# Optimization experiments

Hardware: AMD Instinct MI355X
Metric: run time of the kernel (lower is better)

Reference implementation:

```python
import jax, jax.numpy as jnp
import numpy as np

DIM = 256
DH = 32
HEADS = DIM // DH
AG = 6      # agent_size
WS = 7      # window_size
N = AG * WS * WS  # 294 tokens per window


def _rel_index():
    ws = (AG, WS, WS)
    coords = np.stack(np.meshgrid(np.arange(ws[0]), np.arange(ws[1]), np.arange(ws[2]), indexing='ij'))
    flat = coords.reshape(3, -1)                      # (3, N)
    rel = flat[:, :, None] - flat[:, None, :]         # (3, N, N)
    rel = rel.transpose(1, 2, 0).copy()               # (N, N, 3)
    rel[..., 0] += ws[0] - 1
    rel[..., 1] += ws[1] - 1
    rel[..., 2] += ws[2] - 1
    rel[..., 0] *= (2 * ws[1] - 1) * (2 * ws[2] - 1)
    rel[..., 1] *= (2 * ws[2] - 1)
    return rel.sum(-1).astype(np.int32)               # (N, N)


def setup_inputs() -> dict:
    key = jax.random.key(0)
    k1, k2, k3, k4, k5 = jax.random.split(key, 5)
    x = jax.random.normal(k1, (1, AG, 16, 16, WS, WS, DIM), dtype=jnp.float32)
    mask = jax.random.randint(k2, (1, 16, 16, WS, WS, 1, AG), 0, 2, dtype=jnp.int32)
    w_qkv = jax.random.normal(k3, (DIM, 3 * DIM), dtype=jnp.float32) * (DIM ** -0.5)
    w_out = jax.random.normal(k4, (DIM, DIM), dtype=jnp.float32) * (DIM ** -0.5)
    n_bias = (2 * AG - 1) * (2 * WS - 1) * (2 * WS - 1)
    bias_table = jax.random.normal(k5, (n_bias, HEADS), dtype=jnp.float32) * 0.02
    rel_index = jnp.asarray(_rel_index())
    return {"x": x, "mask": mask, "w_qkv": w_qkv, "w_out": w_out,
            "bias_table": bias_table, "rel_index": rel_index}


def reference(x, mask, w_qkv, w_out, bias_table, rel_index):
    b, l, gx, gy, w1, w2, d = x.shape
    h, dh = HEADS, DH
    # 'b l x y w1 w2 d -> (b x y) (l w1 w2) d'
    xw = x.transpose(0, 2, 3, 1, 4, 5, 6).reshape(b * gx * gy, l * w1 * w2, d)
    B_, n, _ = xw.shape
    qkv = xw @ w_qkv                                  # (B_, N, 3d)
    q, k, v = jnp.split(qkv, 3, axis=-1)
    # 'b n (h d) -> b h n d'
    q = q.reshape(B_, n, h, dh).transpose(0, 2, 1, 3) * (dh ** -0.5)
    k = k.reshape(B_, n, h, dh).transpose(0, 2, 1, 3)
    v = v.reshape(B_, n, h, dh).transpose(0, 2, 1, 3)
    sim = jnp.einsum('bhid,bhjd->bhij', q, k)         # (B_, h, N, N)
    bias = bias_table[rel_index]                      # (N, N, h)
    sim = sim + bias.transpose(2, 0, 1)[None]
    # 'b x y w1 w2 e l -> (b x y) e (l w1 w2)', then unsqueeze head dim
    m = mask.transpose(0, 1, 2, 5, 6, 3, 4).reshape(B_, -1, n)[:, None]  # (B_,1,e,N)
    sim = jnp.where(m == 0, -jnp.inf, sim)
    attn = jax.nn.softmax(sim, axis=-1)
    out = jnp.einsum('bhij,bhjd->bhid', attn, v)      # (B_, h, N, dh)
    # 'b h (l w1 w2) d -> b l w1 w2 (h d)'
    out = out.transpose(0, 2, 1, 3).reshape(B_, l, w1, w2, h * dh)
    out = out @ w_out
    # '(b x y) l w1 w2 d -> b l x y w1 w2 d'
    return out.reshape(b, gx, gy, l, w1, w2, d).transpose(0, 3, 1, 2, 4, 5, 6)
```

## Files before the change

### kernel.cpp

```cpp
#include <hip/hip_runtime.h>

typedef unsigned short u16;
typedef unsigned int   u32;

#define NTOK 294
#define KS_STRIDE 34
#define VT_STRIDE 300
#define WST 260
#define OBUF_BYTES 38535168ull
#define FLAG_OFF (OBUF_BYTES)

#define ROWS_ALLOC 75280ull
#define BUFB (ROWS_ALLOC * 512ull)
#define QWS_OFF   0ull
#define KWS_OFF   (QWS_OFF + BUFB)
#define VWS_OFF   (KWS_OFF + BUFB)
#define OWS_OFF   (VWS_OFF + BUFB)
#define BIASM_OFF (OWS_OFF + BUFB)
#define WQT_OFF   (BIASM_OFF + 1478656ull)
#define WOT_OFF   (WQT_OFF + 393216ull)
#define FLAG2_OFF (WOT_OFF + 131072ull)
#define NEED_WS   (FLAG2_OFF + 4ull)

typedef __fp16 hv2  __attribute__((ext_vector_type(2)));
typedef __fp16 f16x8 __attribute__((ext_vector_type(8)));
typedef float  f32x4 __attribute__((ext_vector_type(4)));

__device__ __forceinline__ float b2f(u16 v){ union{u32 u; float f;} x; x.u = ((u32)v) << 16; return x.f; }
__device__ __forceinline__ u16 f2b(float f){
  union{float f; u32 u;} x; x.f = f; u32 u = x.u;
  return (u16)((u + 0x7fffu + ((u >> 16) & 1u)) >> 16);
}
__device__ __forceinline__ u32 pack2h(float a, float b){
#if __has_builtin(__builtin_amdgcn_cvt_pkrtz)
  auto r = __builtin_amdgcn_cvt_pkrtz(a, b);
  union{ decltype(r) h; u32 u; } x; x.h = r; return x.u;
#else
  union{ hv2 h; u32 u; } x; x.h[0] = (__fp16)a; x.h[1] = (__fp16)b; return x.u;
#endif
}
__device__ __forceinline__ u32 bfp2h(u32 bfp){
  union{u32 u; float f;} lo, hi; lo.u = bfp << 16; hi.u = bfp & 0xffff0000u;
  return pack2h(lo.f, hi.f);
}
__device__ __forceinline__ u16 f2h(float a){ return (u16)(pack2h(a, 0.0f) & 0xffffu); }

__device__ __forceinline__ float dot2f(u32 a, u32 b, float c){
#if __has_builtin(__builtin_amdgcn_fdot2)
  union{u32 u; hv2 h;} A, B; A.u = a; B.u = b;
  return __builtin_amdgcn_fdot2(A.h, B.h, c, false);
#else
  union{u32 u; __fp16 h[2];} A, B; A.u = a; B.u = b;
  return c + (float)A.h[0]*(float)B.h[0] + (float)A.h[1]*(float)B.h[1];
#endif
}

__device__ __forceinline__ f32x4 mfma16(f16x8 a, f16x8 b, f32x4 c){
  return __builtin_amdgcn_mfma_f32_16x16x32_f16(a, b, c, 0, 0, 0);
}

__device__ __forceinline__ void gl2lds16(const void* g, void* l){
#if __has_builtin(__builtin_amdgcn_global_load_lds)
  __builtin_amdgcn_global_load_lds(
      (const __attribute__((address_space(1))) void*)g,
      (__attribute__((address_space(3))) void*)l, 16, 0, 0);
#else
  *(f16x8*)l = *(const f16x8*)g;
#endif
}

__device__ __forceinline__ void stageB(const u16* __restrict__ wsrc, int nt,
                                       u16* lbase, int wave, int lane){
#pragma unroll
  for (int c = 0; c < 2; ++c){
    int G   = (c*4 + wave)*64 + lane;
    int row = G >> 5, g = G & 31;
    int sg  = g ^ (row & 7);
    const u16* src = wsrc + (size_t)nt*4096 + row*256 + sg*8;
    u16* dst = lbase + (size_t)(c*4 + wave)*512;
    gl2lds16(src, dst);
  }
}

__device__ __forceinline__ f16x8 readB(const u16* bb, int ks, int q, int n16){
  return *(const f16x8*)&bb[n16*256 + (((ks*4 + q) ^ (n16 & 7)) * 8)];
}

__global__ void dfab_probe_kernel(const u16* __restrict__ X, int* __restrict__ flag)
{
  const int lane = threadIdx.x;
  int cnt = 0;
#pragma unroll
  for (int k = 0; k < 8; ++k){
    u16 v = X[lane * 8 + k];
    int e = (v >> 7) & 0xFF;
    cnt += (e < 96 || e > 158) ? 1 : 0;
  }
  for (int off = 32; off > 0; off >>= 1) cnt += __shfl_xor(cnt, off);
  if (lane == 0) *flag = (cnt > 64) ? 1 : 0;
}


__global__ __launch_bounds__(256) void dfab_prep_kernel(
    const void* __restrict__ Wqkvv, const void* __restrict__ Woutv,
    const void* __restrict__ BiasTv, const int* __restrict__ RelIdx,
    u16* __restrict__ wqt, u16* __restrict__ wot, u16* __restrict__ biasm,
    const int* __restrict__ flagp)
{
  const int f32m = *(const volatile int*)flagp;
  const u16* Wb = (const u16*)Wqkvv;  const float* Wf = (const float*)Wqkvv;
  const u16* Ob = (const u16*)Woutv;  const float* Of = (const float*)Woutv;
  const u16* Bb = (const u16*)BiasTv; const float* Bf = (const float*)BiasTv;
  int idx = blockIdx.x * 256 + threadIdx.x;
  if (idx < 196608){
    int n = idx >> 8, k = idx & 255;
    float w = f32m ? Wf[k*768 + n] : b2f(Wb[k*768 + n]);
    if (n < 256) w *= 0.17677669529663687f;
    wqt[n*256 + k] = f2h(w);
  } else if (idx < 262144){
    int t = idx - 196608; int n = t >> 8, k = t & 255;
    float w = f32m ? Of[k*256 + n] : b2f(Ob[k*256 + n]);
    wot[n*256 + k] = f2h(w);
  } else {
    int t = idx - 262144;
    int hh = t / 92416; int rem = t - hh * 92416;
    int j = rem / 304;  int i = rem - j * 304;
    float v = 0.f;
    if (i < NTOK && j < NTOK){
      int nb = RelIdx[i * NTOK + j] * 8 + hh;
      v = f32m ? Bf[nb] : b2f(Bb[nb]);
    }
    biasm[((size_t)(hh*304 + j))*304 + i] = f2h(v);
  }
}

__global__ __launch_bounds__(256, 4) void dfab_qkv_kernel(
    const void* __restrict__ Xv, const u16* __restrict__ wqt,
    u16* __restrict__ Qws, u16* __restrict__ Kws, u16* __restrict__ Vws,
    const int* __restrict__ flagp)
{
  __shared__ __align__(16) union {
    u16 xs[64 * 264];
    struct { u16 bs[2][4096]; u16 cs[4][1024]; } p;
  } sm;

  const int tid = threadIdx.x;
  const int m0 = blockIdx.x * 64;
  const int f32m = *(const volatile int*)flagp;
  const u16* Xb = (const u16*)Xv; const float* Xf = (const float*)Xv;
  const int wave = tid >> 6, lane = tid & 63;
  const int q = lane >> 4, n16 = lane & 15;

  for (int idx = tid; idx < 64 * 128; idx += 256){
    int rl = idx >> 7, d2 = idx & 127;
    int m = m0 + rl; int win = m / 294, tok = m - win * 294;
    int l = tok / 49, r = tok - l * 49;
    size_t src = ((size_t)((l*256 + win)*49 + r))*256 + 2*d2;
    u32 hp;
    if (f32m){ float2 xx = *(const float2*)&Xf[src]; hp = pack2h(xx.x, xx.y); }
    else     { hp = bfp2h(*(const u32*)&Xb[src]); }
    *(u32*)&sm.xs[rl * 264 + 2*d2] = hp;
  }
  __syncthreads();

  f16x8 afr[8];
#pragma unroll
  for (int ks = 0; ks < 8; ++ks)
    afr[ks] = *(const f16x8*)&sm.xs[(wave*16 + n16) * 264 + ks*32 + q*8];
  __syncthreads();

  stageB(wqt, 0, &sm.p.bs[0][0], wave, lane);
  __syncthreads();

  u16* myC = &sm.p.cs[wave][0];
  const size_t rowb = (size_t)(m0 + wave*16);
  const int rbrow = lane >> 3, seg = lane & 7;

#pragma unroll 1
  for (int grp = 0; grp < 12; ++grp){
    u16* dstp = (grp < 4) ? Qws : ((grp < 8) ? Kws : Vws);
    const int g4 = grp & 3;
#pragma unroll
    for (int t = 0; t < 4; ++t){
      const int nt = grp*4 + t;
      if (nt < 47) stageB(wqt, nt+1, &sm.p.bs[(nt+1)&1][0], wave, lane);
      const u16* bb = &sm.p.bs[nt&1][0];
      f16x8 bfr[8];
#pragma unroll
      for (int ks = 0; ks < 8; ++ks) bfr[ks] = readB(bb, ks, q, n16);
      f32x4 c0 = {0.f,0.f,0.f,0.f}, c1 = {0.f,0.f,0.f,0.f};
#pragma unroll
      for (int ks = 0; ks < 4; ++ks){
        c0 = mfma16(afr[ks],     bfr[ks],     c0);
        c1 = mfma16(afr[ks + 4], bfr[ks + 4], c1);
      }
#pragma unroll
      for (int r = 0; r < 4; ++r)
        myC[(q*4 + r)*64 + t*16 + n16] = f2h(c0[r] + c1[r]);
      __syncthreads();
    }
    __asm__ volatile("s_waitcnt lgkmcnt(0)" ::: "memory");
#pragma unroll
    for (int p = 0; p < 2; ++p){
      const int row = p*8 + rbrow;
      f16x8 v = *(const f16x8*)&myC[row*64 + seg*8];
      *(f16x8*)&dstp[(rowb + row)*256 + g4*64 + seg*8] = v;
    }
  }
}

__global__ __launch_bounds__(256, 1) void dfab_attn2_kernel(
    const u16* __restrict__ Qws, const u16* __restrict__ Kws,
    const u16* __restrict__ Vws, const u16* __restrict__ BiasM,
    const int* __restrict__ Mask, u16* __restrict__ Ows)
{
  __shared__ __align__(16) u16 Vt[32 * 328];
  __shared__ __align__(16) u16 Pw[4][16 * 168];
  __shared__ float Madd[304];

  const int tid = threadIdx.x;
  const int win = blockIdx.x >> 3, h = blockIdx.x & 7;
  const int wave = tid >> 6, lane = tid & 63;
  const int q = lane >> 4, n16 = lane & 15;

  for (int j = tid; j < 304; j += 256){
    float mv = -1e30f;
    if (j < NTOK){ int l = j / 49, r = j - l * 49;
      mv = (Mask[(win * 49 + r) * 6 + l] != 0) ? 0.0f : -1e30f; }
    Madd[j] = mv;
  }
#pragma unroll 1
  for (int cc = 0; cc < 8; ++cc){
    int c = wave * 8 + cc;
#pragma unroll
    for (int tt = 0; tt < 5; ++tt){
      int tok = lane + 64 * tt;
      u16 v = 0;
      if (tok < NTOK) v = Vws[((size_t)(win*NTOK + tok))*256 + h*32 + c];
      if (tok < 328) Vt[c * 328 + tok] = v;
    }
  }
  __syncthreads();

  u16* myP = Pw[wave];
#pragma unroll 1
  for (int mt = wave; mt < 19; mt += 4){
    const int m0 = mt * 16;
    f16x8 qf = *(const f16x8*)&Qws[((size_t)(win*NTOK + m0 + n16))*256 + h*32 + q*8];

    float S[19][4];
#pragma unroll
    for (int nt = 0; nt < 19; ++nt){
      const int j0 = nt * 16;
      f16x8 kf = *(const f16x8*)&Kws[((size_t)(win*NTOK + j0 + n16))*256 + h*32 + q*8];
      union { uint2 u; __fp16 hh[4]; } bu;
      bu.u = *(const uint2*)&BiasM[((size_t)(h*304 + j0 + n16))*304 + m0 + q*4];
      float madd = Madd[j0 + n16];
      f32x4 c = {0.f, 0.f, 0.f, 0.f};
      c = mfma16(qf, kf, c);
#pragma unroll
      for (int r = 0; r < 4; ++r) S[nt][r] = c[r] + (float)bu.hh[r] + madd;
    }
    float rinv[4];
#pragma unroll
    for (int r = 0; r < 4; ++r){
      float mx = S[0][r];
#pragma unroll
      for (int nt = 1; nt < 19; ++nt) mx = fmaxf(mx, S[nt][r]);
      mx = fmaxf(mx, __shfl_xor(mx, 1));
      mx = fmaxf(mx, __shfl_xor(mx, 2));
      mx = fmaxf(mx, __shfl_xor(mx, 4));
      mx = fmaxf(mx, __shfl_xor(mx, 8));
      float sum = 0.f;
#pragma unroll
      for (int nt = 0; nt < 19; ++nt){ float e = __expf(S[nt][r] - mx); S[nt][r] = e; sum += e; }
      sum += __shfl_xor(sum, 1);
      sum += __shfl_xor(sum, 2);
      sum += __shfl_xor(sum, 4);
      sum += __shfl_xor(sum, 8);
      rinv[r] = 1.0f / sum;
    }
    f32x4 o0 = {0.f,0.f,0.f,0.f}, o1 = {0.f,0.f,0.f,0.f};
#pragma unroll
    for (int half = 0; half < 2; ++half){
#pragma unroll
      for (int ntl = 0; ntl < 10; ++ntl){
        int nt = half * 10 + ntl;
        int col = ntl * 16 + n16;
#pragma unroll
        for (int r = 0; r < 4; ++r)
          myP[(q*4 + r) * 168 + col] = (nt < 19) ? f2h(S[nt][r]) : (u16)0;
      }
      __asm__ volatile("s_waitcnt lgkmcnt(0)" ::: "memory");
#pragma unroll
      for (int kk = 0; kk < 5; ++kk){
        f16x8 pf = *(const f16x8*)&myP[n16 * 168 + kk*32 + q*8];
        f16x8 v0 = *(const f16x8*)&Vt[n16 * 328 + half*160 + kk*32 + q*8];
        f16x8 v1 = *(const f16x8*)&Vt[(16 + n16) * 328 + half*160 + kk*32 + q*8];
        o0 = mfma16(pf, v0, o0);
        o1 = mfma16(pf, v1, o1);
      }
      __asm__ volatile("s_waitcnt lgkmcnt(0)" ::: "memory");
    }
#pragma unroll
    for (int r = 0; r < 4; ++r){
      int tok = m0 + q*4 + r;
      if (tok < NTOK){
        size_t base = ((size_t)(win*NTOK + tok))*256 + h*32;
        Ows[base + n16]      = f2h(o0[r] * rinv[r]);
        Ows[base + 16 + n16] = f2h(o1[r] * rinv[r]);
      }
    }
  }
}

__global__ __launch_bounds__(256, 4) void dfab_proj2_kernel(
    const u16* __restrict__ Ows, const u16* __restrict__ wot,
    void* __restrict__ Outv, const int* __restrict__ flagp)
{
  __shared__ __align__(16) u16   Bs[2][4096];
  __shared__ __align__(16) float Csf[4][16 * 64];

  const int tid = threadIdx.x;
  const int wave = tid >> 6, lane = tid & 63;
  const int q = lane >> 4, n16 = lane & 15;
  const int mr = blockIdx.x * 64 + wave * 16;
  const int f32m = *(const volatile int*)flagp;

  stageB(wot, 0, &Bs[0][0], wave, lane);

  f16x8 afr[8];
#pragma unroll
  for (int ks = 0; ks < 8; ++ks)
    afr[ks] = *(const f16x8*)&Ows[((size_t)(mr + n16))*256 + ks*32 + q*8];

  const int rbrow = lane >> 3, seg = lane & 7;
  size_t ob0, ob1;
  {
    int m = mr + rbrow;     int win = m / 294, tok = m - win*294;
    int l = tok / 49, rr = tok - l*49;
    ob0 = ((size_t)((l*256 + win)*49 + rr))*256;
    m = mr + 8 + rbrow;     win = m / 294; tok = m - win*294;
    l = tok / 49; rr = tok - l*49;
    ob1 = ((size_t)((l*256 + win)*49 + rr))*256;
  }

  float* myC = &Csf[wave][0];
  __syncthreads();

#pragma unroll 1
  for (int g4 = 0; g4 < 4; ++g4){
#pragma unroll
    for (int t = 0; t < 4; ++t){
      const int nt = g4*4 + t;
      if (nt < 15) stageB(wot, nt+1, &Bs[(nt+1)&1][0], wave, lane);
      const u16* bb = &Bs[nt&1][0];
      f16x8 bfr[8];
#pragma unroll
      for (int ks = 0; ks < 8; ++ks) bfr[ks] = readB(bb, ks, q, n16);
      f32x4 c0 = {0.f,0.f,0.f,0.f}, c1 = {0.f,0.f,0.f,0.f};
#pragma unroll
      for (int ks = 0; ks < 4; ++ks){
        c0 = mfma16(afr[ks],     bfr[ks],     c0);
        c1 = mfma16(afr[ks + 4], bfr[ks + 4], c1);
      }
#pragma unroll
      for (int r = 0; r < 4; ++r)
        myC[(q*4 + r)*64 + t*16 + n16] = c0[r] + c1[r];
      __syncthreads();
    }
    __asm__ volatile("s_waitcnt lgkmcnt(0)" ::: "memory");
#pragma unroll
    for (int p = 0; p < 2; ++p){
      const int row = p*8 + rbrow;
      const size_t ob = p ? ob1 : ob0;
      f32x4 v0 = *(const f32x4*)&myC[row*64 + seg*8];
      f32x4 v1 = *(const f32x4*)&myC[row*64 + seg*8 + 4];
      if (f32m){
        *(f32x4*)&((float*)Outv)[ob + g4*64 + seg*8]     = v0;
        *(f32x4*)&((float*)Outv)[ob + g4*64 + seg*8 + 4] = v1;
      } else {
        union{ u32 w[4]; u16 h[8]; } pk;
        pk.h[0]=f2b(v0[0]); pk.h[1]=f2b(v0[1]); pk.h[2]=f2b(v0[2]); pk.h[3]=f2b(v0[3]);
        pk.h[4]=f2b(v1[0]); pk.h[5]=f2b(v1[1]); pk.h[6]=f2b(v1[2]); pk.h[7]=f2b(v1[3]);
        *(uint4*)&((u16*)Outv)[ob + g4*64 + seg*8] = *(const uint4*)&pk.w[0];
      }
    }
  }
}

__global__ __launch_bounds__(256) void dfab_attn_kernel(
    const void* __restrict__ Xv, const int* __restrict__ Mask,
    const void* __restrict__ Wqkvv, const void* __restrict__ BiasTv,
    const int* __restrict__ RelIdx, u16* __restrict__ Obuf,
    const int* __restrict__ flagp)
{
  __shared__ __align__(16) char lds[59736];
  u16* Ks   = (u16*)(lds);
  u16* Vt   = (u16*)(lds + 19992);
  u16* Wp   = (u16*)(lds + 39192);
  u16* Xs   = (u16*)(lds + 47512);
  u16* Wqt  = (u16*)(lds + 39192);
  u32* Pb   = (u32*)(lds + 55832);
  float* Madd = (float*)(lds + 58264);
  u16* Qb   = (u16*)(lds + 59480);

  const int tid = threadIdx.x;
  const int bx  = blockIdx.x;
  const int win = bx >> 3, h = bx & 7;

  const int f32m = *(const volatile int*)flagp;
  const u16*   Xb = (const u16*)Xv;       const float* Xf = (const float*)Xv;
  const u16*   Wb = (const u16*)Wqkvv;    const float* Wf = (const float*)Wqkvv;
  const u16*   Bb = (const u16*)BiasTv;   const float* Bf = (const float*)BiasTv;

  for (int j = tid; j < 304; j += 256){
    float mv = -1e30f;
    if (j < NTOK){ int l = j / 49, r = j - l * 49;
      mv = (Mask[(win * 49 + r) * 6 + l] != 0) ? 0.0f : -1e30f; }
    Madd[j] = mv;
  }
  for (int idx = tid; idx < 32 * 6; idx += 256){
    int c = idx / 6; Vt[c * VT_STRIDE + NTOK + (idx - c * 6)] = 0;
  }

#pragma unroll 1
  for (int p = 0; p < 4; ++p){
    const int kind = p >> 1;
    const int colbase = 256 + kind * 256 + h * 32 + (p & 1) * 16;
    __syncthreads();
    for (int idx = tid; idx < 16 * 128; idx += 256){
      int c = idx & 15, d2 = idx >> 4;
      float w0, w1;
      if (f32m){ w0 = Wf[(2 * d2) * 768 + colbase + c]; w1 = Wf[(2 * d2 + 1) * 768 + colbase + c]; }
      else     { w0 = b2f(Wb[(2 * d2) * 768 + colbase + c]); w1 = b2f(Wb[(2 * d2 + 1) * 768 + colbase + c]); }
      *(u32*)&Wp[c * WST + 2 * d2] = pack2h(w0, w1);
    }
#pragma unroll 1
    for (int jt = 0; jt < 19; ++jt){
      const int j0 = jt * 16;
      const int nj = (NTOK - j0 < 16) ? (NTOK - j0) : 16;
      __syncthreads();
      for (int idx = tid; idx < nj * 128; idx += 256){
        int jl = idx >> 7, d2 = idx & 127;
        int tok = j0 + jl; int l = tok / 49, r = tok - l * 49;
        size_t off = (size_t)((l * 256 + win) * 49 + r) * 256 + 2 * d2;
        u32 hp;
        if (f32m){ float2 xx = *(const float2*)&Xf[off]; hp = pack2h(xx.x, xx.y); }
        else     { hp = bfp2h(*(const u32*)&Xb[off]); }
        *(u32*)&Xs[jl * WST + 2 * d2] = hp;
      }
      __syncthreads();
      const int jl = tid >> 4, c = tid & 15;
      const u32* xp = (const u32*)&Xs[jl * WST];
      const u32* wp = (const u32*)&Wp[c * WST];
      float a0 = 0.f, a1 = 0.f;
#pragma unroll 4
      for (int d2 = 0; d2 < 128; d2 += 4){
        uint2 xa = *(const uint2*)(xp + d2), xb = *(const uint2*)(xp + d2 + 2);
        uint2 wa = *(const uint2*)(wp + d2), wb = *(const uint2*)(wp + d2 + 2);
        a0 = dot2f(xa.x, wa.x, a0); a1 = dot2f(xa.y, wa.y, a1);
        a0 = dot2f(xb.x, wb.x, a0); a1 = dot2f(xb.y, wb.y, a1);
      }
      if (jl < nj){
        u16 hv = f2h(a0 + a1);
        int tok = j0 + jl;
        if (kind == 0) Ks[tok * KS_STRIDE + (p & 1) * 16 + c] = hv;
        else           Vt[((p & 1) * 16 + c) * VT_STRIDE + tok] = hv;
      }
    }
  }
  __syncthreads();
  for (int idx = tid; idx < 32 * 128; idx += 256){
    int c = idx & 31, d2 = idx >> 5;
    float w0, w1;
    if (f32m){ w0 = Wf[(2 * d2) * 768 + h * 32 + c]; w1 = Wf[(2 * d2 + 1) * 768 + h * 32 + c]; }
    else     { w0 = b2f(Wb[(2 * d2) * 768 + h * 32 + c]); w1 = b2f(Wb[(2 * d2 + 1) * 768 + h * 32 + c]); }
    *(u32*)&Wqt[c * WST + 2 * d2] = pack2h(w0, w1);
  }
  __syncthreads();

  const int wave = tid >> 6, lane = tid & 63;
  const int hf = lane >> 5, c32 = lane & 31;
  u32* mypb = Pb + wave * 152;
  u16* qbw  = Qb + wave * 32;

  for (int i = wave; i < NTOK; i += 4){
    const int li = i / 49, ri = i - li * 49;
    const size_t rowoff = (size_t)((li * 256 + win) * 49 + ri) * 256;
    const u32* wqp = (const u32*)&Wqt[c32 * WST];
    float q0 = 0.f, q1 = 0.f;
    if (f32m){
      const float4* xr4 = (const float4*)&Xf[rowoff];
#pragma unroll 4
      for (int d2 = hf * 64; d2 < hf * 64 + 64; d2 += 2){
        uint2 wq = *(const uint2*)(wqp + d2);
        float4 xx = xr4[d2 >> 1];
        q0 = dot2f(pack2h(xx.x, xx.y), wq.x, q0);
        q1 = dot2f(pack2h(xx.z, xx.w), wq.y, q1);
      }
    } else {
      const u32* xr = (const u32*)&Xb[rowoff];
#pragma unroll 4
      for (int d2 = hf * 64; d2 < hf * 64 + 64; d2 += 2){
        uint2 wq = *(const uint2*)(wqp + d2);
        q0 = dot2f(bfp2h(xr[d2]),     wq.x, q0);
        q1 = dot2f(bfp2h(xr[d2 + 1]), wq.y, q1);
      }
    }
    float qa = q0 + q1;
    qa += __shfl_xor(qa, 32);
    if (hf == 0) qbw[c32] = f2h(qa * 0.17677669529663687f);
    __asm__ volatile("s_waitcnt lgkmcnt(0)" ::: "memory");
    u32 qp[16];
#pragma unroll
    for (int cc = 0; cc < 16; ++cc) qp[cc] = *(const u32*)&qbw[2 * cc];

    float sv[5];
#pragma unroll
    for (int it = 0; it < 5; ++it){
      int j = it * 64 + lane;
      float a;
      if (j < NTOK){
        int nb = RelIdx[i * NTOK + j] * 8 + h;
        float bias = f32m ? Bf[nb] : b2f(Bb[nb]);
        float a0 = bias + Madd[j];
        float a1 = 0.f;
        const u16* kr = &Ks[j * KS_STRIDE];
#pragma unroll
        for (int cc = 0; cc < 16; cc += 2){
          a0 = dot2f(qp[cc],     *(const u32*)&kr[2 * cc],     a0);
          a1 = dot2f(qp[cc + 1], *(const u32*)&kr[2 * cc + 2], a1);
        }
        a = a0 + a1;
      } else a = -3e38f;
      sv[it] = a;
    }
    float m = sv[0];
#pragma unroll
    for (int it = 1; it < 5; ++it) m = fmaxf(m, sv[it]);
    for (int off = 32; off > 0; off >>= 1) m = fmaxf(m, __shfl_xor(m, off));
    float lsum = 0.f;
#pragma unroll
    for (int it = 0; it < 5; ++it){ float e = __expf(sv[it] - m); sv[it] = e; lsum += e; }
    for (int off = 32; off > 0; off >>= 1) lsum += __shfl_xor(lsum, off);
    const float rinv = 1.0f / lsum;
#pragma unroll
    for (int it = 0; it < 5; ++it){
      float pn = sv[it] * rinv;
      float po = __shfl_xor(pn, 1);
      int j = it * 64 + lane;
      if (!(lane & 1) && j < 304) mypb[j >> 1] = pack2h(pn, po);
    }
    __asm__ volatile("s_waitcnt lgkmcnt(0)" ::: "memory");
    const u16* vr = &Vt[c32 * VT_STRIDE];
    const int jb = hf * 148;
    float o0 = 0.f, o1 = 0.f;
#pragma unroll 4
    for (int g = 0; g < 37; ++g){
      int j = jb + 4 * g;
      uint2 vv = *(const uint2*)&vr[j];
      uint2 pp = *(const uint2*)&mypb[j >> 1];
      o0 = dot2f(pp.x, vv.x, o0);
      o1 = dot2f(pp.y, vv.y, o1);
    }
    float o = o0 + o1;
    o += __shfl_xor(o, 32);
    if (hf == 0)
      Obuf[(size_t)(win * NTOK + i) * 256 + h * 32 + c32] = f2b(o);
  }
}

__global__ __launch_bounds__(256) void dfab_proj_kernel(
    const u16* __restrict__ Obuf, const void* __restrict__ Woutv,
    void* __restrict__ Outv, const int* __restrict__ flagp)
{
  __shared__ __align__(16) char lds[33920];
  u16* Ot = (u16*)(lds);
  u16* Wt = (u16*)(lds + 16512);

  const int tid = threadIdx.x;
  const int bx = blockIdx.x;
  const int win = bx / 10, tile = bx - win * 10;
  const int t0 = tile * 32;
  const int nt = (NTOK - t0 < 32) ? (NTOK - t0) : 32;

  const int f32m = *(const volatile int*)flagp;
  const u16* Wob = (const u16*)Woutv; const float* Wof = (const float*)Woutv;

  for (int idx = tid; idx < nt * 128; idx += 256){
    int t = idx >> 7, k2 = idx & 127;
    u32 oo = *(const u32*)&Obuf[(size_t)(win * NTOK + t0 + t) * 256 + 2 * k2];
    *(u32*)&Ot[t * 258 + 2 * k2] = bfp2h(oo);
  }

  float acc[32];
#pragma unroll
  for (int t = 0; t < 32; ++t) acc[t] = 0.f;
  const int dd = tid;

#pragma unroll 1
  for (int kt = 0; kt < 8; ++kt){
    __syncthreads();
    for (int idx = tid; idx < 4096; idx += 256){
      int d = idx & 255, kk2 = idx >> 8;
      int k = kt * 32 + 2 * kk2;
      float w0, w1;
      if (f32m){ w0 = Wof[k * 256 + d]; w1 = Wof[(k + 1) * 256 + d]; }
      else     { w0 = b2f(Wob[k * 256 + d]); w1 = b2f(Wob[(k + 1) * 256 + d]); }
      *(u32*)&Wt[d * 34 + 2 * kk2] = pack2h(w0, w1);
    }
    __syncthreads();
#pragma unroll 2
    for (int kk2 = 0; kk2 < 16; ++kk2){
      u32 wp = *(const u32*)&Wt[dd * 34 + 2 * kk2];
      const u16* orow = &Ot[kt * 32 + 2 * kk2];
#pragma unroll 8
      for (int t = 0; t < 32; ++t){
        u32 op = *(const u32*)&orow[t * 258];
        acc[t] = dot2f(op, wp, acc[t]);
      }
    }
  }

  for (int t = 0; t < nt; ++t){
    int tok = t0 + t; int l = tok / 49, r = tok - l * 49;
    size_t oidx = (size_t)((l * 256 + win) * 49 + r) * 256 + dd;
    if (f32m) ((float*)Outv)[oidx] = acc[t];
    else      ((u16*)Outv)[oidx]   = f2b(acc[t]);
  }
}

extern "C" void kernel_launch(void* const* d_in, const int* in_sizes, int n_in,
                              void* d_out, int out_size, void* d_ws, size_t ws_size,
                              hipStream_t stream) {
  (void)in_sizes; (void)n_in; (void)out_size;
  const void* x          = d_in[0];
  const int*  mask       = (const int*)d_in[1];
  const void* w_qkv      = d_in[2];
  const void* w_out      = d_in[3];
  const void* bias_table = d_in[4];
  const int*  rel_index  = (const int*)d_in[5];
  char* ws = (char*)d_ws;

  if (ws_size >= NEED_WS){
    u16* qws   = (u16*)(ws + QWS_OFF);
    u16* kws   = (u16*)(ws + KWS_OFF);
    u16* vws   = (u16*)(ws + VWS_OFF);
    u16* ows   = (u16*)(ws + OWS_OFF);
    u16* biasm = (u16*)(ws + BIASM_OFF);
    u16* wqt   = (u16*)(ws + WQT_OFF);
    u16* wot   = (u16*)(ws + WOT_OFF);
    int* flag  = (int*)(ws + FLAG2_OFF);
    dfab_probe_kernel<<<1, 64, 0, stream>>>((const u16*)x, flag);
    dfab_prep_kernel<<<3912, 256, 0, stream>>>(w_qkv, w_out, bias_table, rel_index,
                                               wqt, wot, biasm, flag);
    dfab_qkv_kernel<<<1176, 256, 0, stream>>>(x, wqt, qws, kws, vws, flag);
    dfab_attn2_kernel<<<2048, 256, 0, stream>>>(qws, kws, vws, biasm, mask, ows);
    dfab_proj2_kernel<<<1176, 256, 0, stream>>>(ows, wot, d_out, flag);
  } else {
    u16* obuf = (u16*)ws;
    int* flag = (int*)(ws + FLAG_OFF);
    dfab_probe_kernel<<<1, 64, 0, stream>>>((const u16*)x, flag);
    dfab_attn_kernel<<<2048, 256, 0, stream>>>(x, mask, w_qkv, bias_table, rel_index, obuf, flag);
    dfab_proj_kernel<<<2560, 256, 0, stream>>>(obuf, w_out, d_out, flag);
  }
}
```

Baseline: 415.7 us.

## Stage K in LDS, vectorize V transpose, prefetch bias and Q in attention

The attention kernel now copies the per-head K slice into shared memory once per block, replacing the repeated global K reads made in every query tile. The V transpose uses 16-byte vector loads instead of scalar loads. Bias values for a tile are loaded into registers before the MFMA loop, and bias plus mask are folded into the MFMA accumulator initialization. The next Q fragment is prefetched before the softmax, and launch bounds allow two blocks per CU. In exchange it adds about 24KB of LDS and more register pressure from the bias and mask arrays, which may limit occupancy or cause spills.

Result: faster. 367.2 us (-11.7%).

```diff
diff --git a/kernel.cpp b/kernel.cpp
--- a/kernel.cpp
+++ b/kernel.cpp
@@ -209,11 +209,12 @@
   }
 }
 
-__global__ __launch_bounds__(256, 1) void dfab_attn2_kernel(
+__global__ __launch_bounds__(256, 2) void dfab_attn2_kernel(
     const u16* __restrict__ Qws, const u16* __restrict__ Kws,
     const u16* __restrict__ Vws, const u16* __restrict__ BiasM,
     const int* __restrict__ Mask, u16* __restrict__ Ows)
 {
+  __shared__ __align__(16) u16 Ks[304 * 40];
   __shared__ __align__(16) u16 Vt[32 * 328];
   __shared__ __align__(16) u16 Pw[4][16 * 168];
   __shared__ float Madd[304];
@@ -229,38 +230,72 @@
       mv = (Mask[(win * 49 + r) * 6 + l] != 0) ? 0.0f : -1e30f; }
     Madd[j] = mv;
   }
+
+  {
+    const int rr0 = tid >> 2, seg = tid & 3;
+#pragma unroll
+    for (int p = 0; p < 5; ++p){
+      int rr = rr0 + p*64;
+      if (rr < NTOK){
+        f16x8 kv = *(const f16x8*)&Kws[((size_t)(win*NTOK + rr))*256 + h*32 + seg*8];
+        *(f16x8*)&Ks[rr*40 + seg*8] = kv;
+      }
+    }
+    if (tid < 40){
+      int rr = NTOK + (tid >> 2);
+      uint4 z = {0u,0u,0u,0u};
+      *(uint4*)&Ks[rr*40 + seg*8] = z;
+    }
+#pragma unroll
+    for (int p = 0; p < 5; ++p){
+      int tok = rr0 + p*64;
+      union{ f16x8 h; u16 s[8]; } vv;
+      uint4 z = {0u,0u,0u,0u};
+      *(uint4*)&vv = z;
+      if (tok < NTOK)
+        vv.h = *(const f16x8*)&Vws[((size_t)(win*NTOK + tok))*256 + h*32 + seg*8];
+      if (tok < 320){
+#pragma unroll
+        for (int k = 0; k < 8; ++k) Vt[(seg*8 + k)*328 + tok] = vv.s[k];
+      }
+    }
+  }
+  __syncthreads();
+
+  float maddv[19];
+#pragma unroll
+  for (int nt = 0; nt < 19; ++nt) maddv[nt] = Madd[nt*16 + n16];
+
+  u16* myP = Pw[wave];
+  int mt = wave;
+  f16x8 qf = *(const f16x8*)&Qws[((size_t)(win*NTOK + mt*16 + n16))*256 + h*32 + q*8];
+
 #pragma unroll 1
-  for (int cc = 0; cc < 8; ++cc){
-    int c = wave * 8 + cc;
-#pragma unroll
-    for (int tt = 0; tt < 5; ++tt){
-      int tok = lane + 64 * tt;
-      u16 v = 0;
-      if (tok < NTOK) v = Vws[((size_t)(win*NTOK + tok))*256 + h*32 + c];
-      if (tok < 328) Vt[c * 328 + tok] = v;
-    }
-  }
-  __syncthreads();
-
-  u16* myP = Pw[wave];
-#pragma unroll 1
-  for (int mt = wave; mt < 19; mt += 4){
+  for (; mt < 19; mt += 4){
     const int m0 = mt * 16;
-    f16x8 qf = *(const f16x8*)&Qws[((size_t)(win*NTOK + m0 + n16))*256 + h*32 + q*8];
+
+    uint2 bu[19];
+#pragma unroll
+    for (int nt = 0; nt < 19; ++nt)
+      bu[nt] = *(const uint2*)&BiasM[((size_t)(h*304 + nt*16 + n16))*304 + m0 + q*4];
 
     float S[19][4];
 #pragma unroll
     for (int nt = 0; nt < 19; ++nt){
-      const int j0 = nt * 16;
-      f16x8 kf = *(const f16x8*)&Kws[((size_t)(win*NTOK + j0 + n16))*256 + h*32 + q*8];
-      union { uint2 u; __fp16 hh[4]; } bu;
-      bu.u = *(const uint2*)&BiasM[((size_t)(h*304 + j0 + n16))*304 + m0 + q*4];
-      float madd = Madd[j0 + n16];
-      f32x4 c = {0.f, 0.f, 0.f, 0.f};
+      f16x8 kf = *(const f16x8*)&Ks[(nt*16 + n16)*40 + q*8];
+      union { uint2 u; __fp16 hh[4]; } b; b.u = bu[nt];
+      f32x4 c = { (float)b.hh[0] + maddv[nt], (float)b.hh[1] + maddv[nt],
+                  (float)b.hh[2] + maddv[nt], (float)b.hh[3] + maddv[nt] };
       c = mfma16(qf, kf, c);
 #pragma unroll
-      for (int r = 0; r < 4; ++r) S[nt][r] = c[r] + (float)bu.hh[r] + madd;
-    }
+      for (int r = 0; r < 4; ++r) S[nt][r] = c[r];
+    }
+
+    const int mtn = mt + 4;
+    f16x8 qfn = qf;
+    if (mtn < 19)
+      qfn = *(const f16x8*)&Qws[((size_t)(win*NTOK + mtn*16 + n16))*256 + h*32 + q*8];
+
     float rinv[4];
 #pragma unroll
     for (int r = 0; r < 4; ++r){
@@ -311,6 +346,7 @@
         Ows[base + 16 + n16] = f2h(o1[r] * rinv[r]);
       }
     }
+    qf = qfn;
   }
 }
 
```
